# Optimization experiments

Measured on AMD Instinct MI355X. Metric: run time of the kernel, lower is better.

Reference implementation:

```python
import jax, jax.numpy as jnp
import numpy as np

B, N, C, S = 4, 65536, 128, 32768
BN = B * N


def setup_inputs() -> dict:
    key = jax.random.key(0)
    k_x, k_perm, k_mask = jax.random.split(key, 3)
    x = jax.random.normal(k_x, (B, N, C), dtype=jnp.float32)
    # every segment non-empty: arange % S, then shuffled over points
    ul_idx = jax.random.permutation(k_perm, jnp.arange(BN, dtype=jnp.int32) % S)
    # representative (first-occurrence) flat point index per segment
    ul_idx_inv = jnp.full((S,), BN, dtype=jnp.int32).at[ul_idx].min(
        jnp.arange(BN, dtype=jnp.int32))
    # gather indices: each point reads its segment's representative location
    rep_flat = ul_idx_inv[ul_idx]  # [BN]
    idx = jnp.stack([rep_flat // N, rep_flat % N], axis=-1).reshape(B, N, 2)
    mask = (jax.random.uniform(k_mask, (B, N, 1)) > 0.1).astype(jnp.float32)
    return {"x": x, "idx": idx, "mask": mask,
            "ul_idx": ul_idx, "ul_idx_inv": ul_idx_inv}


def reference(x, idx, mask, ul_idx, ul_idx_inv):
    b, n, c = x.shape
    xf = x.reshape(b * n, c)                      # [BN, C]
    s = ul_idx_inv.shape[0]
    # unsorted_segment_mean (mode='avg' is what call() uses)
    seg_sum = jax.ops.segment_sum(xf, ul_idx, num_segments=s)          # [S, C]
    cnt = jax.ops.segment_sum(jnp.ones((b * n,), xf.dtype), ul_idx,
                              num_segments=s)                          # [S]
    seg_mean = seg_sum / jnp.maximum(cnt, 1.0)[:, None]
    # scatter_nd segment means to representative point slots
    y = jnp.zeros((b * n, c), xf.dtype).at[ul_idx_inv].set(seg_mean)
    y = y.reshape(b, n, c)
    # gather_nd: each point picks up its cell's pooled feature
    y = y[idx[..., 0], idx[..., 1]]               # [B, N, C]
    return mask * y
```

## Files before the change

kernel.cpp:

```cpp
#include <hip/hip_runtime.h>

#define PB 4
#define PN 65536
#define PC 128
#define PS 32768
#define PBN (PB * PN)

__global__ __launch_bounds__(256) void hist_kernel(
    const int* __restrict__ ul_idx, int* __restrict__ cnt) {
    int p = blockIdx.x * blockDim.x + threadIdx.x;
    if (p < PBN) {
        int s = ul_idx[p];
        if (s >= 0 && s < PS) atomicAdd(&cnt[s], 1);
    }
}

__global__ __launch_bounds__(1024) void scan_kernel(
    const int* __restrict__ cnt,
    int* __restrict__ offsets, int* __restrict__ cursor) {
    __shared__ int partials[1024];
    int t = threadIdx.x;
    int base = t * 32;
    int local[32];
    int sum = 0;
    for (int i = 0; i < 32; i++) { local[i] = cnt[base + i]; sum += local[i]; }
    partials[t] = sum;
    __syncthreads();
    for (int off = 1; off < 1024; off <<= 1) {
        int v = (t >= off) ? partials[t - off] : 0;
        __syncthreads();
        partials[t] += v;
        __syncthreads();
    }
    int excl = (t == 0) ? 0 : partials[t - 1];
    for (int i = 0; i < 32; i++) {
        offsets[base + i] = excl;
        cursor[base + i]  = excl;
        excl += local[i];
    }
}

__global__ __launch_bounds__(256) void plist_kernel(
    const int* __restrict__ ul_idx,
    int* __restrict__ cursor, int* __restrict__ plist) {
    int p = blockIdx.x * blockDim.x + threadIdx.x;
    if (p < PBN) {
        int s = ul_idx[p];
        if (s >= 0 && s < PS) {
            int pos = atomicAdd(&cursor[s], 1);
            plist[pos] = p;
        }
    }
}

__global__ __launch_bounds__(128) void pool_kernel(
    const float* __restrict__ x,
    const int* __restrict__ plist,
    const int* __restrict__ offsets,
    const int* __restrict__ cnt,
    const float* __restrict__ mask,
    float* __restrict__ out) {
    int s = blockIdx.x;
    int c = threadIdx.x;
    int base = offsets[s];
    int n = cnt[s];
    float acc = 0.f;
    for (int i = 0; i < n; i++) {
        int p = plist[base + i];
        acc += x[(size_t)p * PC + c];
    }
    float mean = acc / fmaxf((float)n, 1.f);
    for (int i = 0; i < n; i++) {
        int p = plist[base + i];
        out[(size_t)p * PC + c] = mask[p] * mean;
    }
}

extern "C" void kernel_launch(void* const* d_in, const int* in_sizes, int n_in,
                              void* d_out, int out_size, void* d_ws, size_t ws_size,
                              hipStream_t stream) {
    const float* x      = (const float*)d_in[0];
    const float* mask   = (const float*)d_in[2];
    const int*   ul_idx = (const int*)d_in[3];
    float* out = (float*)d_out;

    int* cnt     = (int*)d_ws;
    int* offsets = cnt + PS;
    int* cursor  = offsets + PS;
    int* plist   = cursor + PS;

    hipMemsetAsync(cnt, 0, PS * sizeof(int), stream);

    const int T = 256;
    hist_kernel <<<(PBN + T - 1) / T, T, 0, stream>>>(ul_idx, cnt);
    scan_kernel <<<1, 1024, 0, stream>>>(cnt, offsets, cursor);
    plist_kernel<<<(PBN + T - 1) / T, T, 0, stream>>>(ul_idx, cursor, plist);
    pool_kernel <<<PS, 128, 0, stream>>>(x, plist, offsets, cnt, mask, out);
}
```

Measured before the change: 305.8 us.

## Parallelize offset scan across blocks and vectorize pooling with float4 per segment

Replaces the single-block 1024-thread scan with a three-kernel hierarchical scan: per-chunk sums, a scan over the chunk bases, then per-chunk exclusive offsets. This spreads the serial prefix work across many blocks. The pool kernel now gives each segment 32 lanes that read and write float4, with 8 segments per block, so memory accesses are wider and there are fewer blocks. It adds two extra kernel launches and a few workspace slots.

```diff
diff --git a/kernel.cpp b/kernel.cpp
--- a/kernel.cpp
+++ b/kernel.cpp
@@ -5,6 +5,9 @@
 #define PC 128
 #define PS 32768
 #define PBN (PB * PN)
+
+#define CHUNK 128
+#define NCHUNK (PS / CHUNK)
 
 __global__ __launch_bounds__(256) void hist_kernel(
     const int* __restrict__ ul_idx, int* __restrict__ cnt) {
@@ -15,29 +18,51 @@
     }
 }
 
-__global__ __launch_bounds__(1024) void scan_kernel(
-    const int* __restrict__ cnt,
-    int* __restrict__ offsets, int* __restrict__ cursor) {
-    __shared__ int partials[1024];
-    int t = threadIdx.x;
-    int base = t * 32;
-    int local[32];
-    int sum = 0;
-    for (int i = 0; i < 32; i++) { local[i] = cnt[base + i]; sum += local[i]; }
-    partials[t] = sum;
+__global__ __launch_bounds__(CHUNK) void chunk_sum_kernel(
+    const int* __restrict__ cnt, int* __restrict__ blk_sum) {
+    __shared__ int sh[CHUNK];
+    int b = blockIdx.x, t = threadIdx.x;
+    sh[t] = cnt[b * CHUNK + t];
     __syncthreads();
-    for (int off = 1; off < 1024; off <<= 1) {
-        int v = (t >= off) ? partials[t - off] : 0;
-        __syncthreads();
-        partials[t] += v;
+    for (int off = CHUNK / 2; off > 0; off >>= 1) {
+        if (t < off) sh[t] += sh[t + off];
         __syncthreads();
     }
-    int excl = (t == 0) ? 0 : partials[t - 1];
-    for (int i = 0; i < 32; i++) {
-        offsets[base + i] = excl;
-        cursor[base + i]  = excl;
-        excl += local[i];
+    if (t == 0) blk_sum[b] = sh[0];
+}
+
+__global__ __launch_bounds__(NCHUNK) void base_scan_kernel(
+    const int* __restrict__ blk_sum, int* __restrict__ blk_base) {
+    __shared__ int sh[NCHUNK];
+    int t = threadIdx.x;
+    sh[t] = blk_sum[t];
+    __syncthreads();
+    for (int off = 1; off < NCHUNK; off <<= 1) {
+        int v = (t >= off) ? sh[t - off] : 0;
+        __syncthreads();
+        sh[t] += v;
+        __syncthreads();
     }
+    blk_base[t] = (t == 0) ? 0 : sh[t - 1];
+}
+
+__global__ __launch_bounds__(CHUNK) void offsets_kernel(
+    const int* __restrict__ cnt, const int* __restrict__ blk_base,
+    int* __restrict__ offsets, int* __restrict__ cursor) {
+    __shared__ int sh[CHUNK];
+    int b = blockIdx.x, t = threadIdx.x;
+    int v = cnt[b * CHUNK + t];
+    sh[t] = v;
+    __syncthreads();
+    for (int off = 1; off < CHUNK; off <<= 1) {
+        int u = (t >= off) ? sh[t - off] : 0;
+        __syncthreads();
+        sh[t] += u;
+        __syncthreads();
+    }
+    int excl = blk_base[b] + sh[t] - v;
+    offsets[b * CHUNK + t] = excl;
+    cursor[b * CHUNK + t]  = excl;
 }
 
 __global__ __launch_bounds__(256) void plist_kernel(
@@ -53,26 +78,31 @@
     }
 }
 
-__global__ __launch_bounds__(128) void pool_kernel(
+__global__ __launch_bounds__(256) void pool_kernel(
     const float* __restrict__ x,
     const int* __restrict__ plist,
     const int* __restrict__ offsets,
     const int* __restrict__ cnt,
     const float* __restrict__ mask,
     float* __restrict__ out) {
-    int s = blockIdx.x;
-    int c = threadIdx.x;
+    int t = threadIdx.x;
+    int lane = t & 31;
+    int s = blockIdx.x * 8 + (t >> 5);
     int base = offsets[s];
     int n = cnt[s];
-    float acc = 0.f;
+    float4 acc = make_float4(0.f, 0.f, 0.f, 0.f);
     for (int i = 0; i < n; i++) {
         int p = plist[base + i];
-        acc += x[(size_t)p * PC + c];
+        float4 v = ((const float4*)(x + (size_t)p * PC))[lane];
+        acc.x += v.x; acc.y += v.y; acc.z += v.z; acc.w += v.w;
     }
-    float mean = acc / fmaxf((float)n, 1.f);
+    float inv = 1.f / fmaxf((float)n, 1.f);
+    float4 mean = make_float4(acc.x * inv, acc.y * inv, acc.z * inv, acc.w * inv);
     for (int i = 0; i < n; i++) {
         int p = plist[base + i];
-        out[(size_t)p * PC + c] = mask[p] * mean;
+        float m = mask[p];
+        float4 r = make_float4(mean.x * m, mean.y * m, mean.z * m, mean.w * m);
+        ((float4*)(out + (size_t)p * PC))[lane] = r;
     }
 }
 
@@ -84,16 +114,20 @@
     const int*   ul_idx = (const int*)d_in[3];
     float* out = (float*)d_out;
 
-    int* cnt     = (int*)d_ws;
-    int* offsets = cnt + PS;
-    int* cursor  = offsets + PS;
-    int* plist   = cursor + PS;
+    int* cnt      = (int*)d_ws;
+    int* offsets  = cnt + PS;
+    int* cursor   = offsets + PS;
+    int* blk_sum  = cursor + PS;
+    int* blk_base = blk_sum + NCHUNK;
+    int* plist    = blk_base + NCHUNK;
 
     hipMemsetAsync(cnt, 0, PS * sizeof(int), stream);
 
     const int T = 256;
-    hist_kernel <<<(PBN + T - 1) / T, T, 0, stream>>>(ul_idx, cnt);
-    scan_kernel <<<1, 1024, 0, stream>>>(cnt, offsets, cursor);
-    plist_kernel<<<(PBN + T - 1) / T, T, 0, stream>>>(ul_idx, cursor, plist);
-    pool_kernel <<<PS, 128, 0, stream>>>(x, plist, offsets, cnt, mask, out);
+    hist_kernel     <<<(PBN + T - 1) / T, T, 0, stream>>>(ul_idx, cnt);
+    chunk_sum_kernel<<<NCHUNK, CHUNK, 0, stream>>>(cnt, blk_sum);
+    base_scan_kernel<<<1, NCHUNK, 0, stream>>>(blk_sum, blk_base);
+    offsets_kernel  <<<NCHUNK, CHUNK, 0, stream>>>(cnt, blk_base, offsets, cursor);
+    plist_kernel    <<<(PBN + T - 1) / T, T, 0, stream>>>(ul_idx, cursor, plist);
+    pool_kernel     <<<PS / 8, T, 0, stream>>>(x, plist, offsets, cnt, mask, out);
 }
```

After: 286.2 us. 6.4% less time.
